# Performance work log

Hardware: AMD Instinct MI355X
Metric: run time of the kernel (lower is better)

## Reference

```python
import jax, jax.numpy as jnp
import numpy as np

NUM_HOPS = 4
N_NODES = 50000
N_EDGES = 500000
D = 128
H1 = 256
INIT_A, INIT_B = -0.01, 0.01


def _mlp(x, w1, b1, w2, b2):
    # Linear -> ReLU -> Linear -> ReLU (Dropout is identity in eval mode)
    h = jax.nn.relu(x @ w1 + b1)
    return jax.nn.relu(h @ w2 + b2)


def _uniform(key, shape):
    return jax.random.uniform(key, shape, jnp.float32, INIT_A, INIT_B)


def setup_inputs() -> dict:
    key = jax.random.key(0)
    ks = jax.random.split(key, 40)
    inp = {
        "batch_token": jax.random.normal(ks[0], (N_NODES, D), jnp.float32),
        "edge_p_node": jax.random.randint(ks[1], (N_EDGES,), 0, N_NODES),
        "edge_c_node": jax.random.randint(ks[2], (N_EDGES,), 0, N_NODES),
        "edge_p_indicate": jax.random.uniform(ks[3], (N_EDGES,), jnp.float32),
        "edge_c_indicate": jax.random.uniform(ks[4], (N_EDGES,), jnp.float32),
        "p_mask": jax.random.uniform(ks[5], (N_NODES,), jnp.float32),
        "c_mask": jax.random.uniform(ks[6], (N_NODES,), jnp.float32),
        "start_token": jax.random.normal(ks[7], (D,), jnp.float32),
        "end_token": jax.random.normal(ks[8], (D,), jnp.float32),
    }
    # MLP_V: D -> H1 -> D ; MLP_E: 1 -> H1 -> D ; MLP_p/c/aggr: 3D -> H1 -> D
    k = 9
    for name, din in (("V", D), ("E", 1), ("P", 3 * D), ("C", 3 * D), ("A", 3 * D)):
        inp[name + "w1"] = _uniform(ks[k], (din, H1)); k += 1
        inp[name + "b1"] = _uniform(ks[k], (H1,)); k += 1
        inp[name + "w2"] = _uniform(ks[k], (H1, D)); k += 1
        inp[name + "b2"] = _uniform(ks[k], (D,)); k += 1
    return inp


def reference(batch_token, edge_p_node, edge_c_node, edge_p_indicate,
              edge_c_indicate, p_mask, c_mask, start_token, end_token,
              Vw1, Vb1, Vw2, Vb2, Ew1, Eb1, Ew2, Eb2,
              Pw1, Pb1, Pw2, Pb2, Cw1, Cb1, Cw2, Cb2,
              Aw1, Ab1, Aw2, Ab2):
    n = batch_token.shape[0]
    h = _mlp(batch_token, Vw1, Vb1, Vw2, Vb2)  # [N, D]
    edge_p = _mlp(edge_p_indicate[:, None], Ew1, Eb1, Ew2, Eb2)  # [E, D]
    edge_c = _mlp(edge_c_indicate[:, None], Ew1, Eb1, Ew2, Eb2)  # [E, D]
    ones_e = jnp.ones((edge_p_node.shape[0],), jnp.float32)
    cnt_p = jnp.clip(jax.ops.segment_sum(ones_e, edge_p_node, num_segments=n), 1.0)
    cnt_c = jnp.clip(jax.ops.segment_sum(ones_e, edge_c_node, num_segments=n), 1.0)
    for _ in range(NUM_HOPS - 1):
        hp = h[edge_p_node]  # [E, D]
        hc = h[edge_c_node]  # [E, D]
        s_p = _mlp(jnp.concatenate([hc, hp, edge_p], -1), Pw1, Pb1, Pw2, Pb2)
        s_c = _mlp(jnp.concatenate([hp, hc, edge_c], -1), Cw1, Cb1, Cw2, Cb2)
        s_p = jax.ops.segment_sum(s_p, edge_p_node, num_segments=n) / cnt_p[:, None]
        s_c = jax.ops.segment_sum(s_c, edge_c_node, num_segments=n) / cnt_c[:, None]
        s_p = s_p + p_mask[:, None] * start_token
        s_c = s_c + c_mask[:, None] * end_token
        x_aggr = jnp.concatenate([h, s_p, s_c], -1)  # [N, 3D]
        h = jax.nn.relu(h + _mlp(x_aggr, Aw1, Ab1, Aw2, Ab2))
    return h
```

## Files before the change

kernel.cpp:

```cpp
#include <hip/hip_runtime.h>
#include <hip/hip_bf16.h>
#include <cstdint>
#include <cstddef>
#include <cmath>

typedef __bf16 bf16;
typedef bf16 bf16x8 __attribute__((ext_vector_type(8)));
typedef float f32x4 __attribute__((ext_vector_type(4)));

#define D_DIM 128
#define NB 32
#define EB 64
#define TS 136
#define XS 264
#define SRS 132
#define AS 392

__device__ __forceinline__ f32x4 mfma16(bf16x8 a, bf16x8 b, f32x4 c) {
  return __builtin_amdgcn_mfma_f32_16x16x32_bf16(a, b, c, 0, 0, 0);
}

__device__ __forceinline__ int clampi(int v, int hi) {
  return v < 0 ? 0 : (v > hi ? hi : v);
}

__device__ __forceinline__ void stage16(const float* __restrict__ src, bf16* dst) {
  bf16 tmp[16];
#pragma unroll
  for (int q = 0; q < 4; ++q) {
    f32x4 f = ((const f32x4*)src)[q];
#pragma unroll
    for (int j = 0; j < 4; ++j) tmp[q * 4 + j] = (bf16)f[j];
  }
  *(bf16x8*)dst = *(bf16x8*)tmp;
  *(bf16x8*)(dst + 8) = *(bf16x8*)(tmp + 8);
}

template <int NSEG>
__device__ __forceinline__ void mlp_layer1(const bf16* s0, const bf16* s1, const bf16* s2,
                                           const int S,
                                           const bf16* __restrict__ W1t,
                                           const float* __restrict__ B1,
                                           bf16* x2, const int lane, const int w) {
  const int col = lane & 15, quad = lane >> 4;
  const int K = NSEG * 128;
  f32x4 acc[2][4] = {};
  const bf16* segs[3] = {s0, s1, s2};
#pragma unroll
  for (int sg = 0; sg < NSEG; ++sg) {
    const bf16* xl = segs[sg];
#pragma unroll
    for (int kk = 0; kk < 128; kk += 32) {
      const int k0 = sg * 128 + kk;
      bf16x8 a0 = *(const bf16x8*)&xl[col * S + kk + quad * 8];
      bf16x8 a1 = *(const bf16x8*)&xl[(col + 16) * S + kk + quad * 8];
#pragma unroll
      for (int nt = 0; nt < 4; ++nt) {
        bf16x8 b = *(const bf16x8*)(W1t + (size_t)(w * 64 + nt * 16 + col) * K + k0 + quad * 8);
        acc[0][nt] = mfma16(a0, b, acc[0][nt]);
        acc[1][nt] = mfma16(a1, b, acc[1][nt]);
      }
    }
  }
#pragma unroll
  for (int nt = 0; nt < 4; ++nt) {
    const int n = w * 64 + nt * 16 + col;
    const float b1 = B1[n];
#pragma unroll
    for (int mt = 0; mt < 2; ++mt)
#pragma unroll
      for (int i = 0; i < 4; ++i) {
        float v = acc[mt][nt][i] + b1;
        x2[(mt * 16 + quad * 4 + i) * XS + n] = (bf16)(v > 0.f ? v : 0.f);
      }
  }
}

__device__ __forceinline__ void mlp_layer2(const bf16* x2, const bf16* __restrict__ W2t,
                                           const int lane, const int w, f32x4 acc2[2][2]) {
  const int col = lane & 15, quad = lane >> 4;
#pragma unroll
  for (int k0 = 0; k0 < 256; k0 += 32) {
    bf16x8 a0 = *(const bf16x8*)&x2[col * XS + k0 + quad * 8];
    bf16x8 a1 = *(const bf16x8*)&x2[(col + 16) * XS + k0 + quad * 8];
#pragma unroll
    for (int nt = 0; nt < 2; ++nt) {
      bf16x8 b = *(const bf16x8*)(W2t + (size_t)(w * 32 + nt * 16 + col) * 256 + k0 + quad * 8);
      acc2[0][nt] = mfma16(a0, b, acc2[0][nt]);
      acc2[1][nt] = mfma16(a1, b, acc2[1][nt]);
    }
  }
}

__device__ __forceinline__ void emit_z(const bf16* x, const int S,
                                       const bf16* __restrict__ Pw1t,
                                       const bf16* __restrict__ Cw1t,
                                       bf16* __restrict__ Zbuf,
                                       const int r0, const int N,
                                       const int lane, const int w) {
  const int col = lane & 15, quad = lane >> 4;
  const bf16* base = ((w & 2) ? Cw1t : Pw1t) + (w & 1) * 128;
  bf16* out = Zbuf + (size_t)w * ((size_t)N * 256);
#pragma unroll
  for (int half = 0; half < 2; ++half) {
    f32x4 acc[2][8] = {};
#pragma unroll
    for (int kc = 0; kc < 4; ++kc) {
      bf16x8 a0 = *(const bf16x8*)&x[col * S + kc * 32 + quad * 8];
      bf16x8 a1 = *(const bf16x8*)&x[(col + 16) * S + kc * 32 + quad * 8];
#pragma unroll
      for (int nt = 0; nt < 8; ++nt) {
        const int n = half * 128 + nt * 16 + col;
        bf16x8 b = *(const bf16x8*)(base + (size_t)n * 384 + kc * 32 + quad * 8);
        acc[0][nt] = mfma16(a0, b, acc[0][nt]);
        acc[1][nt] = mfma16(a1, b, acc[1][nt]);
      }
    }
#pragma unroll
    for (int nt = 0; nt < 8; ++nt) {
      const int n = half * 128 + nt * 16 + col;
#pragma unroll
      for (int mt = 0; mt < 2; ++mt)
#pragma unroll
        for (int i = 0; i < 4; ++i) {
          int g = r0 + mt * 16 + quad * 4 + i;
          if (g < N) out[(size_t)g * 256 + n] = (bf16)acc[mt][nt][i];
        }
    }
  }
}


__global__ void transpose_kernel(const float* __restrict__ in, bf16* __restrict__ out,
                                 int K, int N) {
  int k = blockIdx.x * blockDim.x + threadIdx.x;
  int n = blockIdx.y;
  if (k < K) out[(size_t)n * K + k] = (bf16)in[(size_t)k * N + n];
}

__global__ void count_kernel(const int* __restrict__ epn, const int* __restrict__ ecn,
                             int* cntp, int* cntc, int E, int N) {
  int i = blockIdx.x * blockDim.x + threadIdx.x;
  if (i < E) {
    atomicAdd(&cntp[clampi(epn[i], N - 1)], 1);
    atomicAdd(&cntc[clampi(ecn[i], N - 1)], 1);
  }
}

__global__ void inv_kernel(const int* __restrict__ cntp, const int* __restrict__ cntc,
                           float* invp, float* invc, int N) {
  int i = blockIdx.x * blockDim.x + threadIdx.x;
  if (i < N) {
    invp[i] = 1.f / fmaxf((float)cntp[i], 1.f);
    invc[i] = 1.f / fmaxf((float)cntc[i], 1.f);
  }
}

__global__ void scan_pair_kernel(const int* __restrict__ cntp, const int* __restrict__ cntc,
                                 int* __restrict__ offp, int* __restrict__ offc, int n) {
  const int* cnt = blockIdx.x ? cntc : cntp;
  int* offs = blockIdx.x ? offc : offp;
  __shared__ int buf[1024];
  __shared__ int carry;
  const int t = threadIdx.x;
  if (t == 0) carry = 0;
  __syncthreads();
  for (int base = 0; base < n; base += 1024) {
    int v = (base + t < n) ? cnt[base + t] : 0;
    buf[t] = v;
    __syncthreads();
    for (int d = 1; d < 1024; d <<= 1) {
      int add = (t >= d) ? buf[t - d] : 0;
      __syncthreads();
      buf[t] += add;
      __syncthreads();
    }
    if (base + t < n) offs[base + t] = carry + buf[t] - v;
    __syncthreads();
    if (t == 1023) carry += buf[1023];
    __syncthreads();
  }
}

__global__ void scatter_kernel(const int* __restrict__ epn, const int* __restrict__ ecn,
                               const int* __restrict__ offp, const int* __restrict__ offc,
                               int* curp, int* curc, int* sortp, int* sortc, int E, int N) {
  int i = blockIdx.x * blockDim.x + threadIdx.x;
  if (i < E) {
    int p = clampi(epn[i], N - 1);
    sortp[offp[p] + atomicAdd(&curp[p], 1)] = i;
    int c = clampi(ecn[i], N - 1);
    sortc[offc[c] + atomicAdd(&curc[c], 1)] = i;
  }
}


__global__ __launch_bounds__(256) void emlp_table_kernel(
    const float* __restrict__ Ew1, const float* __restrict__ Eb1,
    const float* __restrict__ Ew2, const float* __restrict__ Eb2,
    float* __restrict__ ts_out, float* __restrict__ Atab, float* __restrict__ Btab) {
  __shared__ float s_tk[256], s_w[256], s_b[256];
  __shared__ int s_k[256];
  __shared__ float sA[256], sB[256];
  const int j = blockIdx.x;
  const int t = threadIdx.x;
  float w = Ew1[t], b = Eb1[t];
  float tk = (w != 0.f) ? (-b / w) : INFINITY;
  s_tk[t] = tk; s_w[t] = w; s_b[t] = b;
  __syncthreads();
  int rank = 0;
  for (int u = 0; u < 256; ++u) {
    float tu = s_tk[u];
    if (tu < tk || (tu == tk && u < t)) ++rank;
  }
  s_k[rank] = t;
  if (j == 0) ts_out[rank] = tk;
  float w2own = Ew2[(size_t)t * 128 + j];
  bool act = (w < 0.f || (w == 0.f && b > 0.f));
  sA[t] = act ? w * w2own : 0.f;
  sB[t] = act ? b * w2own : 0.f;
  __syncthreads();
  for (int d = 128; d > 0; d >>= 1) {
    if (t < d) { sA[t] += sA[t + d]; sB[t] += sB[t + d]; }
    __syncthreads();
  }
  const float baseA = sA[0], baseB = sB[0];
  __syncthreads();
  int k = s_k[t];
  float wk = s_w[k], bk = s_b[k];
  float dA = 0.f, dB = 0.f;
  if (wk != 0.f) {
    float w2 = Ew2[(size_t)k * 128 + j];
    float sgn = wk > 0.f ? 1.f : -1.f;
    dA = sgn * wk * w2;
    dB = sgn * bk * w2;
  }
  sA[t] = dA; sB[t] = dB;
  __syncthreads();
  for (int d = 1; d < 256; d <<= 1) {
    float aA = (t >= d) ? sA[t - d] : 0.f;
    float aB = (t >= d) ? sB[t - d] : 0.f;
    __syncthreads();
    sA[t] += aA; sB[t] += aB;
    __syncthreads();
  }
  const float eb2 = Eb2[j];
  if (t == 0) { Atab[j] = baseA; Btab[j] = baseB + eb2; }
  Atab[(size_t)(t + 1) * 128 + j] = baseA + sA[t];
  Btab[(size_t)(t + 1) * 128 + j] = baseB + sB[t] + eb2;
}


__global__ __launch_bounds__(256, 3) void node_v_kernel(
    const float* __restrict__ bt, const bf16* __restrict__ W1t, const float* __restrict__ B1,
    const bf16* __restrict__ W2t, const float* __restrict__ B2,
    const bf16* __restrict__ Pw1t, const bf16* __restrict__ Cw1t,
    bf16* __restrict__ Zbuf, float* __restrict__ hout, int N) {
  __shared__ __attribute__((aligned(16))) bf16 x[NB * TS];
  __shared__ __attribute__((aligned(16))) bf16 x2[NB * XS];
  const int t = threadIdx.x;
  const int r0 = blockIdx.x * NB;
  {
    const int r = t >> 3, c0 = (t & 7) * 16;
    int g = r0 + r; if (g >= N) g = N - 1;
    stage16(bt + (size_t)g * D_DIM + c0, &x[r * TS + c0]);
  }
  __syncthreads();
  const int lane = t & 63, w = t >> 6, col = lane & 15, quad = lane >> 4;
  mlp_layer1<1>(x, x, x, TS, W1t, B1, x2, lane, w);
  __syncthreads();
  f32x4 acc2[2][2] = {};
  mlp_layer2(x2, W2t, lane, w, acc2);
  __syncthreads();
#pragma unroll
  for (int nt = 0; nt < 2; ++nt) {
    const int n = w * 32 + nt * 16 + col;
    const float b2 = B2[n];
#pragma unroll
    for (int mt = 0; mt < 2; ++mt)
#pragma unroll
      for (int i = 0; i < 4; ++i) {
        int m = mt * 16 + quad * 4 + i;
        int g = r0 + m;
        float v = acc2[mt][nt][i] + b2;
        v = v > 0.f ? v : 0.f;
        x[m * TS + n] = (bf16)v;
        if (g < N) hout[(size_t)g * D_DIM + n] = v;
      }
  }
  __syncthreads();
  emit_z(x, TS, Pw1t, Cw1t, Zbuf, r0, N, lane, w);
}


__global__ __launch_bounds__(512, 8) void edge_side_kernel(
    const bf16* __restrict__ Zbuf,
    const float* __restrict__ epi, const float* __restrict__ eci,
    const int* __restrict__ epn, const int* __restrict__ ecn,
    const int* __restrict__ sortp, const int* __restrict__ sortc,
    const float* __restrict__ ets, const float* __restrict__ Atab,
    const float* __restrict__ Btab,
    const bf16* __restrict__ Pw1t, const float* __restrict__ Pb1,
    const bf16* __restrict__ Pw2t, const float* __restrict__ Pb2,
    const bf16* __restrict__ Cw1t, const float* __restrict__ Cb1,
    const bf16* __restrict__ Cw2t, const float* __restrict__ Cb2,
    float* __restrict__ accp, float* __restrict__ accc, int E, int N) {
  const int side = blockIdx.y;
  const size_t NZ = (size_t)N * 256;
  const bf16* ZO     = Zbuf + (size_t)(side * 2 + 0) * NZ;
  const bf16* ZW     = Zbuf + (size_t)(side * 2 + 1) * NZ;
  const float* ei    = side ? eci : epi;
  const int* own_n   = side ? ecn : epn;
  const int* oth_n   = side ? epn : ecn;
  const int* sorted  = side ? sortc : sortp;
  const bf16* W1c    = (side ? Cw1t : Pw1t) + 256;
  const float* B1    = side ? Cb1 : Pb1;
  const bf16* W2t    = side ? Cw2t : Pw2t;
  const float* B2    = side ? Cb2 : Pb2;
  float* acc         = side ? accc : accp;

  __shared__ int s_own[EB], s_oth[EB];
  __shared__ float s_x[EB];
  __shared__ float s_ts[256];
  __shared__ __attribute__((aligned(16))) char ubuf[EB * TS * 2 * 2];
  bf16* feat = (bf16*)ubuf;
  bf16* xzh  = (bf16*)(ubuf + EB * TS * 2);
  float* sred = (float*)ubuf;

  const int t = threadIdx.x;
  const int e0 = blockIdx.x * EB;
  if (t < 256) s_ts[t] = ets[t];
  if (t < EB) {
    int e = e0 + t;
    if (e < E) {
      int id = clampi(sorted[e], E - 1);
      s_own[t] = clampi(own_n[id], N - 1);
      s_oth[t] = clampi(oth_n[id], N - 1);
      s_x[t] = ei[id];
    } else {
      s_own[t] = -1; s_oth[t] = 0; s_x[t] = 0.f;
    }
  }
  __syncthreads();

  const int lane = t & 63, w = t >> 6, col = lane & 15, quad = lane >> 4;
  const int zr = t >> 3, zc = (t & 7) * 16;

  const bf16* zo_row;
  const bf16* zw_row;
  bf16x8 va0, va1;
  {
    int ro = s_oth[zr];
    int rw = s_own[zr]; if (rw < 0) rw = 0;
    zo_row = ZO + (size_t)ro * 256;
    zw_row = ZW + (size_t)rw * 256;
    va0 = *(const bf16x8*)(zo_row + zc);
    va1 = *(const bf16x8*)(zo_row + zc + 8);
  }

  {
    const float xv = s_x[zr];
    int lo = 0, hi = 256;
#pragma unroll
    for (int it = 0; it < 8; ++it) {
      int mid = (lo + hi) >> 1;
      if (s_ts[mid] < xv) lo = mid + 1; else hi = mid;
    }
    const float* Ar = Atab + (size_t)lo * 128 + zc;
    const float* Br = Btab + (size_t)lo * 128 + zc;
#pragma unroll
    for (int q = 0; q < 2; ++q) {
      f32x4 a0 = *(const f32x4*)(Ar + q * 8);
      f32x4 a1 = *(const f32x4*)(Ar + q * 8 + 4);
      f32x4 b0 = *(const f32x4*)(Br + q * 8);
      f32x4 b1v = *(const f32x4*)(Br + q * 8 + 4);
      bf16 o[8];
#pragma unroll
      for (int j = 0; j < 4; ++j) {
        float v0 = fmaf(xv, a0[j], b0[j]);
        float v1 = fmaf(xv, a1[j], b1v[j]);
        o[j] = (bf16)(v0 > 0.f ? v0 : 0.f);
        o[4 + j] = (bf16)(v1 > 0.f ? v1 : 0.f);
      }
      *(bf16x8*)&feat[zr * TS + zc + q * 8] = *(bf16x8*)o;
    }
  }

  {
    bf16x8 b0 = *(const bf16x8*)(zw_row + zc);
    bf16x8 b1 = *(const bf16x8*)(zw_row + zc + 8);
    bf16 o0[8], o1[8];
#pragma unroll
    for (int j = 0; j < 8; ++j) {
      o0[j] = (bf16)((float)va0[j] + (float)b0[j]);
      o1[j] = (bf16)((float)va1[j] + (float)b1[j]);
    }
    *(bf16x8*)&xzh[zr * TS + zc] = *(bf16x8*)o0;
    *(bf16x8*)&xzh[zr * TS + zc + 8] = *(bf16x8*)o1;
  }
  __syncthreads();

  va0 = *(const bf16x8*)(zo_row + 128 + zc);
  va1 = *(const bf16x8*)(zo_row + 128 + zc + 8);

  f32x4 acc2[4];
#pragma unroll
  for (int g = 0; g < 4; ++g) acc2[g] = (f32x4){0.f, 0.f, 0.f, 0.f};

  const int nh = w * 16 + col;

  {
    f32x4 acc1[4] = {};
#pragma unroll
    for (int kc = 0; kc < 4; ++kc) {
      bf16x8 afr[4];
#pragma unroll
      for (int g = 0; g < 4; ++g)
        afr[g] = *(const bf16x8*)&feat[(g * 16 + col) * TS + kc * 32 + quad * 8];
      bf16x8 b = *(const bf16x8*)(W1c + (size_t)nh * 384 + kc * 32 + quad * 8);
#pragma unroll
      for (int g = 0; g < 4; ++g) acc1[g] = mfma16(afr[g], b, acc1[g]);
    }
    const float b1v = B1[nh];
#pragma unroll
    for (int g = 0; g < 4; ++g)
#pragma unroll
      for (int i = 0; i < 4; ++i) {
        const int m = g * 16 + quad * 4 + i;
        float v = acc1[g][i] + b1v + (float)xzh[m * TS + nh];
        xzh[m * TS + nh] = (bf16)(v > 0.f ? v : 0.f);
      }
  }
  __syncthreads();
#pragma unroll
  for (int kc = 0; kc < 4; ++kc) {
    bf16x8 afr[4];
#pragma unroll
    for (int g = 0; g < 4; ++g)
      afr[g] = *(const bf16x8*)&xzh[(g * 16 + col) * TS + kc * 32 + quad * 8];
    bf16x8 b = *(const bf16x8*)(W2t + (size_t)nh * 256 + kc * 32 + quad * 8);
#pragma unroll
    for (int g = 0; g < 4; ++g) acc2[g] = mfma16(afr[g], b, acc2[g]);
  }
  __syncthreads();

  {
    bf16x8 b0 = *(const bf16x8*)(zw_row + 128 + zc);
    bf16x8 b1 = *(const bf16x8*)(zw_row + 128 + zc + 8);
    bf16 o0[8], o1[8];
#pragma unroll
    for (int j = 0; j < 8; ++j) {
      o0[j] = (bf16)((float)va0[j] + (float)b0[j]);
      o1[j] = (bf16)((float)va1[j] + (float)b1[j]);
    }
    *(bf16x8*)&xzh[zr * TS + zc] = *(bf16x8*)o0;
    *(bf16x8*)&xzh[zr * TS + zc + 8] = *(bf16x8*)o1;
  }
  __syncthreads();

  {
    f32x4 acc1[4] = {};
#pragma unroll
    for (int kc = 0; kc < 4; ++kc) {
      bf16x8 afr[4];
#pragma unroll
      for (int g = 0; g < 4; ++g)
        afr[g] = *(const bf16x8*)&feat[(g * 16 + col) * TS + kc * 32 + quad * 8];
      bf16x8 b = *(const bf16x8*)(W1c + (size_t)(128 + nh) * 384 + kc * 32 + quad * 8);
#pragma unroll
      for (int g = 0; g < 4; ++g) acc1[g] = mfma16(afr[g], b, acc1[g]);
    }
    const float b1v = B1[128 + nh];
#pragma unroll
    for (int g = 0; g < 4; ++g)
#pragma unroll
      for (int i = 0; i < 4; ++i) {
        const int m = g * 16 + quad * 4 + i;
        float v = acc1[g][i] + b1v + (float)xzh[m * TS + nh];
        xzh[m * TS + nh] = (bf16)(v > 0.f ? v : 0.f);
      }
  }
  __syncthreads();
#pragma unroll
  for (int kc = 0; kc < 4; ++kc) {
    bf16x8 afr[4];
#pragma unroll
    for (int g = 0; g < 4; ++g)
      afr[g] = *(const bf16x8*)&xzh[(g * 16 + col) * TS + kc * 32 + quad * 8];
    bf16x8 b = *(const bf16x8*)(W2t + (size_t)nh * 256 + 128 + kc * 32 + quad * 8);
#pragma unroll
    for (int g = 0; g < 4; ++g) acc2[g] = mfma16(afr[g], b, acc2[g]);
  }
  __syncthreads();

  {
    const float b2 = B2[nh];
#pragma unroll
    for (int g = 0; g < 4; ++g)
#pragma unroll
      for (int i = 0; i < 4; ++i) {
        float v = acc2[g][i] + b2;
        sred[(g * 16 + quad * 4 + i) * SRS + nh] = v > 0.f ? v : 0.f;
      }
  }
  __syncthreads();
  {
    const int c = w * 16 + (lane >> 2);
    const int rlo = (lane & 3) * 16;
    float run = 0.f;
    int cur = s_own[rlo];
    for (int r = rlo; r < rlo + 16; ++r) {
      int k = s_own[r];
      if (k != cur) {
        if (cur >= 0)
          __hip_atomic_fetch_add(&acc[(size_t)cur * D_DIM + c], run,
                                 __ATOMIC_RELAXED, __HIP_MEMORY_SCOPE_AGENT);
        run = 0.f;
        cur = k;
      }
      run += sred[r * SRS + c];
    }
    if (cur >= 0)
      __hip_atomic_fetch_add(&acc[(size_t)cur * D_DIM + c], run,
                             __ATOMIC_RELAXED, __HIP_MEMORY_SCOPE_AGENT);
  }
}


__global__ __launch_bounds__(256, 3) void node_a_kernel(
    const float* __restrict__ h, const float* __restrict__ accp, const float* __restrict__ accc,
    const float* __restrict__ invp, const float* __restrict__ invc,
    const float* __restrict__ pmask, const float* __restrict__ cmask,
    const float* __restrict__ stok, const float* __restrict__ etok,
    const bf16* __restrict__ W1t, const float* __restrict__ B1,
    const bf16* __restrict__ W2t, const float* __restrict__ B2,
    const bf16* __restrict__ Pw1t, const bf16* __restrict__ Cw1t,
    bf16* __restrict__ Zbuf, int emitZ,
    float* __restrict__ hout, int N) {
  __shared__ __attribute__((aligned(16))) bf16 x[NB * AS];
  __shared__ __attribute__((aligned(16))) bf16 x2[NB * XS];
  const int t = threadIdx.x;
  const int r0 = blockIdx.x * NB;
  {
    const int r = t >> 3, c0 = (t & 7) * 16;
    int g = r0 + r; if (g >= N) g = N - 1;
    stage16(h + (size_t)g * D_DIM + c0, &x[r * AS + c0]);
  }
  {
    const int j = t;
    for (int r = 0; r < NB; ++r) {
      int g = r0 + r; if (g >= N) g = N - 1;
      float v;
      if (j < 128)
        v = accp[(size_t)g * D_DIM + j] * invp[g] + pmask[g] * stok[j];
      else {
        int jj = j - 128;
        v = accc[(size_t)g * D_DIM + jj] * invc[g] + cmask[g] * etok[jj];
      }
      x[r * AS + 128 + j] = (bf16)v;
    }
  }
  __syncthreads();
  const int lane = t & 63, w = t >> 6, col = lane & 15, quad = lane >> 4;
  mlp_layer1<3>(x, x + 128, x + 256, AS, W1t, B1, x2, lane, w);
  __syncthreads();
  f32x4 acc2[2][2] = {};
  mlp_layer2(x2, W2t, lane, w, acc2);
  __syncthreads();
#pragma unroll
  for (int nt = 0; nt < 2; ++nt) {
    const int n = w * 32 + nt * 16 + col;
    const float b2 = B2[n];
#pragma unroll
    for (int mt = 0; mt < 2; ++mt)
#pragma unroll
      for (int i = 0; i < 4; ++i) {
        int m = mt * 16 + quad * 4 + i;
        int g = r0 + m;
        int gc = g < N ? g : N - 1;
        float mlpv = acc2[mt][nt][i] + b2;
        mlpv = mlpv > 0.f ? mlpv : 0.f;
        float v = h[(size_t)gc * D_DIM + n] + mlpv;
        v = v > 0.f ? v : 0.f;
        x[m * AS + n] = (bf16)v;
        if (g < N) hout[(size_t)g * D_DIM + n] = v;
      }
  }
  if (emitZ) {
    __syncthreads();
    emit_z(x, AS, Pw1t, Cw1t, Zbuf, r0, N, lane, w);
  }
}


extern "C" void kernel_launch(void* const* d_in, const int* in_sizes, int n_in,
                              void* d_out, int out_size, void* d_ws, size_t ws_size,
                              hipStream_t stream) {
  const float* batch_token = (const float*)d_in[0];
  const int* epn = (const int*)d_in[1];
  const int* ecn = (const int*)d_in[2];
  const float* epi = (const float*)d_in[3];
  const float* eci = (const float*)d_in[4];
  const float* pmask = (const float*)d_in[5];
  const float* cmask = (const float*)d_in[6];
  const float* stok = (const float*)d_in[7];
  const float* etok = (const float*)d_in[8];
  const float *Vw1 = (const float*)d_in[9], *Vb1 = (const float*)d_in[10],
              *Vw2 = (const float*)d_in[11], *Vb2 = (const float*)d_in[12];
  const float *Ew1 = (const float*)d_in[13], *Eb1 = (const float*)d_in[14],
              *Ew2 = (const float*)d_in[15], *Eb2 = (const float*)d_in[16];
  const float *Pw1 = (const float*)d_in[17], *Pb1 = (const float*)d_in[18],
              *Pw2 = (const float*)d_in[19], *Pb2 = (const float*)d_in[20];
  const float *Cw1 = (const float*)d_in[21], *Cb1 = (const float*)d_in[22],
              *Cw2 = (const float*)d_in[23], *Cb2 = (const float*)d_in[24];
  const float *Aw1 = (const float*)d_in[25], *Ab1 = (const float*)d_in[26],
              *Aw2 = (const float*)d_in[27], *Ab2 = (const float*)d_in[28];
  const int N = in_sizes[5];
  const int E = in_sizes[1];

  char* ws = (char*)d_ws;
  size_t off = 0;
  auto alloc = [&](size_t bytes) {
    size_t o = off;
    off += (bytes + 511) & ~(size_t)511;
    return o;
  };
  float* accp = (float*)(ws + alloc((size_t)N * D_DIM * 4));
  float* accc = (float*)(ws + alloc((size_t)N * D_DIM * 4));
  bf16* Zbuf = (bf16*)(ws + alloc((size_t)4 * N * 256 * 2));
  float* invp = (float*)(ws + alloc((size_t)N * 4));
  float* invc = (float*)(ws + alloc((size_t)N * 4));
  int* cntp = (int*)(ws + alloc((size_t)N * 4));
  int* cntc = (int*)(ws + alloc((size_t)N * 4));
  int* offp = (int*)(ws + alloc((size_t)N * 4));
  int* offc = (int*)(ws + alloc((size_t)N * 4));
  int* curp = (int*)(ws + alloc((size_t)N * 4));
  int* curc = (int*)(ws + alloc((size_t)N * 4));
  int* sortp = (int*)(ws + alloc((size_t)E * 4));
  int* sortc = (int*)(ws + alloc((size_t)E * 4));
  bf16* Vw1t = (bf16*)(ws + alloc(128 * 256 * 2));
  bf16* Pw1t = (bf16*)(ws + alloc(384 * 256 * 2));
  bf16* Cw1t = (bf16*)(ws + alloc(384 * 256 * 2));
  bf16* Aw1t = (bf16*)(ws + alloc(384 * 256 * 2));
  bf16* Vw2t = (bf16*)(ws + alloc(256 * 128 * 2));
  bf16* Pw2t = (bf16*)(ws + alloc(256 * 128 * 2));
  bf16* Cw2t = (bf16*)(ws + alloc(256 * 128 * 2));
  bf16* Aw2t = (bf16*)(ws + alloc(256 * 128 * 2));
  float* ets  = (float*)(ws + alloc(256 * 4));
  float* Atab = (float*)(ws + alloc((size_t)257 * 128 * 4));
  float* Btab = (float*)(ws + alloc((size_t)257 * 128 * 4));
  float* hbuf = (float*)d_out;
  (void)ws_size; (void)n_in; (void)out_size;

  const dim3 blk(256);
  transpose_kernel<<<dim3(1, 256), blk, 0, stream>>>(Vw1, Vw1t, 128, 256);
  transpose_kernel<<<dim3(2, 256), blk, 0, stream>>>(Pw1, Pw1t, 384, 256);
  transpose_kernel<<<dim3(2, 256), blk, 0, stream>>>(Cw1, Cw1t, 384, 256);
  transpose_kernel<<<dim3(2, 256), blk, 0, stream>>>(Aw1, Aw1t, 384, 256);
  transpose_kernel<<<dim3(1, 128), blk, 0, stream>>>(Vw2, Vw2t, 256, 128);
  transpose_kernel<<<dim3(1, 128), blk, 0, stream>>>(Pw2, Pw2t, 256, 128);
  transpose_kernel<<<dim3(1, 128), blk, 0, stream>>>(Cw2, Cw2t, 256, 128);
  transpose_kernel<<<dim3(1, 128), blk, 0, stream>>>(Aw2, Aw2t, 256, 128);

  emlp_table_kernel<<<dim3(128), dim3(256), 0, stream>>>(Ew1, Eb1, Ew2, Eb2, ets, Atab, Btab);

  const size_t cntbytes = (size_t)((char*)(cntc + N) - (char*)cntp);
  hipMemsetAsync(cntp, 0, cntbytes, stream);
  count_kernel<<<dim3((E + 255) / 256), blk, 0, stream>>>(epn, ecn, cntp, cntc, E, N);
  inv_kernel<<<dim3((N + 255) / 256), blk, 0, stream>>>(cntp, cntc, invp, invc, N);
  scan_pair_kernel<<<dim3(2), dim3(1024), 0, stream>>>(cntp, cntc, offp, offc, N);
  const size_t curbytes = (size_t)((char*)(curc + N) - (char*)curp);
  hipMemsetAsync(curp, 0, curbytes, stream);
  scatter_kernel<<<dim3((E + 255) / 256), blk, 0, stream>>>(epn, ecn, offp, offc,
                                                            curp, curc, sortp, sortc, E, N);

  const int nblocks = (N + NB - 1) / NB;
  const int eblocks = (E + EB - 1) / EB;

  node_v_kernel<<<dim3(nblocks), blk, 0, stream>>>(
      batch_token, Vw1t, Vb1, Vw2t, Vb2, Pw1t, Cw1t, Zbuf, hbuf, N);

  const size_t accbytes = (size_t)((char*)(accc + (size_t)N * D_DIM) - (char*)accp);
  for (int hop = 0; hop < 3; ++hop) {
    hipMemsetAsync(accp, 0, accbytes, stream);
    edge_side_kernel<<<dim3(eblocks, 2), dim3(512), 0, stream>>>(
        Zbuf, epi, eci, epn, ecn, sortp, sortc, ets, Atab, Btab,
        Pw1t, Pb1, Pw2t, Pb2, Cw1t, Cb1, Cw2t, Cb2, accp, accc, E, N);
    node_a_kernel<<<dim3(nblocks), blk, 0, stream>>>(
        hbuf, accp, accc, invp, invc, pmask, cmask, stok, etok,
        Aw1t, Ab1, Aw2t, Ab2, Pw1t, Cw1t, Zbuf, (hop < 2) ? 1 : 0, hbuf, N);
  }
}
```

Measured before the change: 2.052 ms.

## Double edge tile to 128 edges per block in edge-side MLP kernel

Raises the edge tile from 64 to 128 edges per block, so each wave computes 8 row-groups of MFMA per weight fragment instead of 4. The goal is to halve global weight loads per edge and improve weight reuse, and sorted-edge segment runs get longer so fewer atomics are issued. Gather threads now cover 32 columns each, and the reduction is remapped so each thread sums 32 rows for one column. The costs are larger shared-memory tiles, more accumulator registers, and a launch bound lowered to 4 blocks per CU, which reduces occupancy.

```diff
diff --git a/kernel.cpp b/kernel.cpp
--- a/kernel.cpp
+++ b/kernel.cpp
@@ -10,7 +10,7 @@
 
 #define D_DIM 128
 #define NB 32
-#define EB 64
+#define EB 128
 #define TS 136
 #define XS 264
 #define SRS 132
@@ -293,7 +293,7 @@
 }
 
 
-__global__ __launch_bounds__(512, 8) void edge_side_kernel(
+__global__ __launch_bounds__(512, 4) void edge_side_kernel(
     const bf16* __restrict__ Zbuf,
     const float* __restrict__ epi, const float* __restrict__ eci,
     const int* __restrict__ epn, const int* __restrict__ ecn,
@@ -344,18 +344,18 @@
   __syncthreads();
 
   const int lane = t & 63, w = t >> 6, col = lane & 15, quad = lane >> 4;
-  const int zr = t >> 3, zc = (t & 7) * 16;
+  const int zr = t >> 2, zc = (t & 3) * 32;
 
   const bf16* zo_row;
   const bf16* zw_row;
-  bf16x8 va0, va1;
+  bf16x8 va[4];
   {
     int ro = s_oth[zr];
     int rw = s_own[zr]; if (rw < 0) rw = 0;
     zo_row = ZO + (size_t)ro * 256;
     zw_row = ZW + (size_t)rw * 256;
-    va0 = *(const bf16x8*)(zo_row + zc);
-    va1 = *(const bf16x8*)(zo_row + zc + 8);
+#pragma unroll
+    for (int q = 0; q < 4; ++q) va[q] = *(const bf16x8*)(zo_row + zc + q * 8);
   }
 
   {
@@ -369,7 +369,7 @@
     const float* Ar = Atab + (size_t)lo * 128 + zc;
     const float* Br = Btab + (size_t)lo * 128 + zc;
 #pragma unroll
-    for (int q = 0; q < 2; ++q) {
+    for (int q = 0; q < 4; ++q) {
       f32x4 a0 = *(const f32x4*)(Ar + q * 8);
       f32x4 a1 = *(const f32x4*)(Ar + q * 8 + 4);
       f32x4 b0 = *(const f32x4*)(Br + q * 8);
@@ -387,43 +387,40 @@
   }
 
   {
-    bf16x8 b0 = *(const bf16x8*)(zw_row + zc);
-    bf16x8 b1 = *(const bf16x8*)(zw_row + zc + 8);
-    bf16 o0[8], o1[8];
-#pragma unroll
-    for (int j = 0; j < 8; ++j) {
-      o0[j] = (bf16)((float)va0[j] + (float)b0[j]);
-      o1[j] = (bf16)((float)va1[j] + (float)b1[j]);
-    }
-    *(bf16x8*)&xzh[zr * TS + zc] = *(bf16x8*)o0;
-    *(bf16x8*)&xzh[zr * TS + zc + 8] = *(bf16x8*)o1;
-  }
-  __syncthreads();
-
-  va0 = *(const bf16x8*)(zo_row + 128 + zc);
-  va1 = *(const bf16x8*)(zo_row + 128 + zc + 8);
-
-  f32x4 acc2[4];
-#pragma unroll
-  for (int g = 0; g < 4; ++g) acc2[g] = (f32x4){0.f, 0.f, 0.f, 0.f};
+#pragma unroll
+    for (int q = 0; q < 4; ++q) {
+      bf16x8 b = *(const bf16x8*)(zw_row + zc + q * 8);
+      bf16 o[8];
+#pragma unroll
+      for (int j = 0; j < 8; ++j) o[j] = (bf16)((float)va[q][j] + (float)b[j]);
+      *(bf16x8*)&xzh[zr * TS + zc + q * 8] = *(bf16x8*)o;
+    }
+  }
+  __syncthreads();
+
+#pragma unroll
+  for (int q = 0; q < 4; ++q) va[q] = *(const bf16x8*)(zo_row + 128 + zc + q * 8);
+
+  f32x4 acc2[8];
+#pragma unroll
+  for (int g = 0; g < 8; ++g) acc2[g] = (f32x4){0.f, 0.f, 0.f, 0.f};
 
   const int nh = w * 16 + col;
 
   {
-    f32x4 acc1[4] = {};
+    f32x4 acc1[8] = {};
 #pragma unroll
     for (int kc = 0; kc < 4; ++kc) {
-      bf16x8 afr[4];
-#pragma unroll
-      for (int g = 0; g < 4; ++g)
-        afr[g] = *(const bf16x8*)&feat[(g * 16 + col) * TS + kc * 32 + quad * 8];
       bf16x8 b = *(const bf16x8*)(W1c + (size_t)nh * 384 + kc * 32 + quad * 8);
 #pragma unroll
-      for (int g = 0; g < 4; ++g) acc1[g] = mfma16(afr[g], b, acc1[g]);
+      for (int g = 0; g < 8; ++g) {
+        bf16x8 afr = *(const bf16x8*)&feat[(g * 16 + col) * TS + kc * 32 + quad * 8];
+        acc1[g] = mfma16(afr, b, acc1[g]);
+      }
     }
     const float b1v = B1[nh];
 #pragma unroll
-    for (int g = 0; g < 4; ++g)
+    for (int g = 0; g < 8; ++g)
 #pragma unroll
       for (int i = 0; i < 4; ++i) {
         const int m = g * 16 + quad * 4 + i;
@@ -434,45 +431,41 @@
   __syncthreads();
 #pragma unroll
   for (int kc = 0; kc < 4; ++kc) {
-    bf16x8 afr[4];
-#pragma unroll
-    for (int g = 0; g < 4; ++g)
-      afr[g] = *(const bf16x8*)&xzh[(g * 16 + col) * TS + kc * 32 + quad * 8];
     bf16x8 b = *(const bf16x8*)(W2t + (size_t)nh * 256 + kc * 32 + quad * 8);
 #pragma unroll
-    for (int g = 0; g < 4; ++g) acc2[g] = mfma16(afr[g], b, acc2[g]);
-  }
-  __syncthreads();
-
-  {
-    bf16x8 b0 = *(const bf16x8*)(zw_row + 128 + zc);
-    bf16x8 b1 = *(const bf16x8*)(zw_row + 128 + zc + 8);
-    bf16 o0[8], o1[8];
-#pragma unroll
-    for (int j = 0; j < 8; ++j) {
-      o0[j] = (bf16)((float)va0[j] + (float)b0[j]);
-      o1[j] = (bf16)((float)va1[j] + (float)b1[j]);
-    }
-    *(bf16x8*)&xzh[zr * TS + zc] = *(bf16x8*)o0;
-    *(bf16x8*)&xzh[zr * TS + zc + 8] = *(bf16x8*)o1;
-  }
-  __syncthreads();
-
-  {
-    f32x4 acc1[4] = {};
+    for (int g = 0; g < 8; ++g) {
+      bf16x8 afr = *(const bf16x8*)&xzh[(g * 16 + col) * TS + kc * 32 + quad * 8];
+      acc2[g] = mfma16(afr, b, acc2[g]);
+    }
+  }
+  __syncthreads();
+
+  {
+#pragma unroll
+    for (int q = 0; q < 4; ++q) {
+      bf16x8 b = *(const bf16x8*)(zw_row + 128 + zc + q * 8);
+      bf16 o[8];
+#pragma unroll
+      for (int j = 0; j < 8; ++j) o[j] = (bf16)((float)va[q][j] + (float)b[j]);
+      *(bf16x8*)&xzh[zr * TS + zc + q * 8] = *(bf16x8*)o;
+    }
+  }
+  __syncthreads();
+
+  {
+    f32x4 acc1[8] = {};
 #pragma unroll
     for (int kc = 0; kc < 4; ++kc) {
-      bf16x8 afr[4];
-#pragma unroll
-      for (int g = 0; g < 4; ++g)
-        afr[g] = *(const bf16x8*)&feat[(g * 16 + col) * TS + kc * 32 + quad * 8];
       bf16x8 b = *(const bf16x8*)(W1c + (size_t)(128 + nh) * 384 + kc * 32 + quad * 8);
 #pragma unroll
-      for (int g = 0; g < 4; ++g) acc1[g] = mfma16(afr[g], b, acc1[g]);
+      for (int g = 0; g < 8; ++g) {
+        bf16x8 afr = *(const bf16x8*)&feat[(g * 16 + col) * TS + kc * 32 + quad * 8];
+        acc1[g] = mfma16(afr, b, acc1[g]);
+      }
     }
     const float b1v = B1[128 + nh];
 #pragma unroll
-    for (int g = 0; g < 4; ++g)
+    for (int g = 0; g < 8; ++g)
 #pragma unroll
       for (int i = 0; i < 4; ++i) {
         const int m = g * 16 + quad * 4 + i;
@@ -483,20 +476,19 @@
   __syncthreads();
 #pragma unroll
   for (int kc = 0; kc < 4; ++kc) {
-    bf16x8 afr[4];
-#pragma unroll
-    for (int g = 0; g < 4; ++g)
-      afr[g] = *(const bf16x8*)&xzh[(g * 16 + col) * TS + kc * 32 + quad * 8];
     bf16x8 b = *(const bf16x8*)(W2t + (size_t)nh * 256 + 128 + kc * 32 + quad * 8);
 #pragma unroll
-    for (int g = 0; g < 4; ++g) acc2[g] = mfma16(afr[g], b, acc2[g]);
+    for (int g = 0; g < 8; ++g) {
+      bf16x8 afr = *(const bf16x8*)&xzh[(g * 16 + col) * TS + kc * 32 + quad * 8];
+      acc2[g] = mfma16(afr, b, acc2[g]);
+    }
   }
   __syncthreads();
 
   {
     const float b2 = B2[nh];
 #pragma unroll
-    for (int g = 0; g < 4; ++g)
+    for (int g = 0; g < 8; ++g)
 #pragma unroll
       for (int i = 0; i < 4; ++i) {
         float v = acc2[g][i] + b2;
@@ -505,11 +497,11 @@
   }
   __syncthreads();
   {
-    const int c = w * 16 + (lane >> 2);
-    const int rlo = (lane & 3) * 16;
+    const int c = t & 127;
+    const int rlo = (t >> 7) * 32;
     float run = 0.f;
     int cur = s_own[rlo];
-    for (int r = rlo; r < rlo + 16; ++r) {
+    for (int r = rlo; r < rlo + 32; ++r) {
       int k = s_own[r];
       if (k != cur) {
         if (cur >= 0)
```

Measured after the change: 2.006 ms. 1.02x faster.
